# Performance work log

Hardware: AMD Instinct MI355X
Metric: run time of the kernel (lower is better)

Reference implementation:

```python
import jax, jax.numpy as jnp
import numpy as np

DIM = 2048
N_HEADS = 16
N_KV_HEADS = 8
HEAD_DIM = DIM // N_HEADS  # 128
N_REP = N_HEADS // N_KV_HEADS
BATCH = 2
SEQ = 2048
CHUNK = 128  # chunked-parallel causal linear attention; SEQ % CHUNK == 0


def _make_freqs_cis(seq_len, head_dim, theta=10000.0):
    freqs = 1.0 / (theta ** (np.arange(0, head_dim, 2, dtype=np.float32) / head_dim))
    t = np.arange(seq_len, dtype=np.float32)
    ang = np.outer(t, freqs)  # [S, D/2]
    return jnp.asarray(np.stack([np.cos(ang), np.sin(ang)], axis=-1))  # [S, D/2, 2]


def setup_inputs() -> dict:
    key = jax.random.key(0)
    ks = jax.random.split(key, 5)
    x = jax.random.normal(ks[0], (BATCH, SEQ, DIM), dtype=jnp.float32)
    freqs_cis = _make_freqs_cis(SEQ, HEAD_DIM)
    s = 0.02
    wq = s * jax.random.normal(ks[1], (N_HEADS * HEAD_DIM, DIM), dtype=jnp.float32)
    wk = s * jax.random.normal(ks[2], (N_KV_HEADS * HEAD_DIM, DIM), dtype=jnp.float32)
    wv = s * jax.random.normal(ks[3], (N_KV_HEADS * HEAD_DIM, DIM), dtype=jnp.float32)
    wo = s * jax.random.normal(ks[4], (DIM, N_HEADS * HEAD_DIM), dtype=jnp.float32)
    return {"x": x, "freqs_cis": freqs_cis, "wq": wq, "wk": wk, "wv": wv, "wo": wo}


def _apply_rotary(x, freqs_cis):
    # x: [B, S, H, D]; freqs_cis: [S, D/2, 2] (cos, sin). Llama pairing: (x0,x1),(x2,x3),...
    B, S, H, D = x.shape
    xr = x.reshape(B, S, H, D // 2, 2)
    x0, x1 = xr[..., 0], xr[..., 1]
    c = freqs_cis[None, :, None, :, 0]
    s = freqs_cis[None, :, None, :, 1]
    o0 = x0 * c - x1 * s
    o1 = x0 * s + x1 * c
    return jnp.stack([o0, o1], axis=-1).reshape(B, S, H, D)


def _causal_linear_attention(q, k, v):
    # q, k, v: [B, H, S, D]; output_i = q_i @ sum_{j<=i} k_j^T v_j
    B, H, S, D = q.shape
    q = jax.nn.softmax(q * (D ** -0.5), axis=-1)  # softmax over feature dim
    k = jax.nn.softmax(k, axis=2)                 # softmax over sequence dim (as in source)
    Nc = S // CHUNK
    qc = q.reshape(B, H, Nc, CHUNK, D)
    kc = k.reshape(B, H, Nc, CHUNK, D)
    vc = v.reshape(B, H, Nc, CHUNK, D)
    # per-chunk KV outer-product sums: [B, H, Nc, D, D]
    kv = jnp.einsum('bhncd,bhnce->bhnde', kc, vc)
    cum = jnp.cumsum(kv, axis=2)
    cum_excl = jnp.concatenate([jnp.zeros_like(cum[:, :, :1]), cum[:, :, :-1]], axis=2)
    inter = jnp.einsum('bhncd,bhnde->bhnce', qc, cum_excl)
    scores = jnp.einsum('bhncd,bhnmd->bhncm', qc, kc)  # [B,H,Nc,C,C]
    mask = jnp.tril(jnp.ones((CHUNK, CHUNK), dtype=bool))
    scores = jnp.where(mask, scores, jnp.zeros((), dtype=scores.dtype))
    intra = jnp.einsum('bhncm,bhnme->bhnce', scores, vc)
    return (inter + intra).reshape(B, H, S, D)


def reference(x, freqs_cis, wq, wk, wv, wo):
    B, S, _ = x.shape
    xq = (x @ wq.T).reshape(B, S, N_HEADS, HEAD_DIM)
    xk = (x @ wk.T).reshape(B, S, N_KV_HEADS, HEAD_DIM)
    xv = (x @ wv.T).reshape(B, S, N_KV_HEADS, HEAD_DIM)
    xq = _apply_rotary(xq, freqs_cis)
    xk = _apply_rotary(xk, freqs_cis)
    # repeat_kv: each kv head repeated N_REP consecutive times
    keys = jnp.repeat(xk, N_REP, axis=2)
    values = jnp.repeat(xv, N_REP, axis=2)
    q = jnp.transpose(xq, (0, 2, 1, 3))
    k = jnp.transpose(keys, (0, 2, 1, 3))
    v = jnp.transpose(values, (0, 2, 1, 3))
    out = _causal_linear_attention(q, k, v)  # [B, H, S, D]
    out = jnp.transpose(out, (0, 2, 1, 3)).reshape(B, S, N_HEADS * HEAD_DIM)
    return out @ wo.T
```

## Files before the change

kernel.cpp:

```cpp
#include <hip/hip_runtime.h>
#include <math.h>

#define DIMV 2048
#define NHEAD 16
#define NKV 8
#define HD 128
#define BATCH 2
#define SEQ 2048
#define CHUNK 128
#define NCHUNK 16
#define MTOK 4096
#define KVD (NKV * HD)

typedef _Float16 half8_t __attribute__((ext_vector_type(8)));
typedef _Float16 half4_t __attribute__((ext_vector_type(4)));
typedef _Float16 half2_t __attribute__((ext_vector_type(2)));
typedef float f32x4 __attribute__((ext_vector_type(4)));

#define GLOBAL_AS __attribute__((address_space(1)))
#define LDS_AS __attribute__((address_space(3)))

#define BARX() __builtin_amdgcn_s_barrier()
#define WAITL(n) asm volatile("s_waitcnt lgkmcnt(" #n ")" ::: "memory")
#define WAITVM(n) asm volatile("s_waitcnt vmcnt(" #n ")" ::: "memory")

__global__ __launch_bounds__(256) void cast_all(const float* __restrict__ x,
                                                const float* __restrict__ wq,
                                                const float* __restrict__ wk,
                                                const float* __restrict__ wv,
                                                const float* __restrict__ wo,
                                                _Float16* __restrict__ xh,
                                                _Float16* __restrict__ wqkvh,
                                                _Float16* __restrict__ woh) {
  long i = (long)(blockIdx.x * 256 + threadIdx.x) * 8;
  const float* src;
  _Float16* dst;
  long off;
  if (i < 8388608)        { src = x;  dst = xh;              off = 0; }
  else if (i < 12582912)  { src = wq; dst = wqkvh;           off = 8388608; }
  else if (i < 14680064)  { src = wk; dst = wqkvh + 4194304; off = 12582912; }
  else if (i < 16777216)  { src = wv; dst = wqkvh + 6291456; off = 14680064; }
  else                    { src = wo; dst = woh;             off = 16777216; }
  long e = i - off;
  float4 a = *(const float4*)&src[e];
  float4 b = *(const float4*)&src[e + 4];
  half8_t h = {(_Float16)a.x, (_Float16)a.y, (_Float16)a.z, (_Float16)a.w,
               (_Float16)b.x, (_Float16)b.y, (_Float16)b.z, (_Float16)b.w};
  *(half8_t*)&dst[e] = h;
}

__global__ __launch_bounds__(256) void transpose_fc(const float* __restrict__ fc,
                                                    float* __restrict__ fcT) {
  __shared__ float T[64][65];
  int s0 = blockIdx.x * 64, d0 = blockIdx.y * 64;
  int t = threadIdx.x;
  int r = t >> 4, c4 = (t & 15) * 4;
#pragma unroll
  for (int p = 0; p < 4; ++p) {
    int sr = p * 16 + r;
    float4 v = *(const float4*)&fc[(size_t)(s0 + sr) * 128 + d0 + c4];
    T[sr][c4] = v.x; T[sr][c4 + 1] = v.y; T[sr][c4 + 2] = v.z; T[sr][c4 + 3] = v.w;
  }
  __syncthreads();
#pragma unroll
  for (int p = 0; p < 4; ++p) {
    int dr = p * 16 + r;
    float4 v = make_float4(T[c4][dr], T[c4 + 1][dr], T[c4 + 2][dr], T[c4 + 3][dr]);
    *(float4*)&fcT[(size_t)(d0 + dr) * SEQ + s0 + c4] = v;
  }
}

#define STG_A(bb, kk, i, k0)                                                      \
  __builtin_amdgcn_global_load_lds(                                               \
      (const GLOBAL_AS void*)(A + aoff + (size_t)(i) * 128 * 2048 + (k0) + (kk) * 32), \
      (LDS_AS void*)(As + ((bb) * 2 + (kk)) * 8192 + (i) * 4096 + wave * 512), 16, 0, 0)
#define STG_B(bb, kk, i, k0)                                                      \
  __builtin_amdgcn_global_load_lds(                                               \
      (const GLOBAL_AS void*)(B + boff + (size_t)(i) * 128 * 2048 + (k0) + (kk) * 32), \
      (LDS_AS void*)(Bs + ((bb) * 2 + (kk)) * 8192 + (i) * 4096 + wave * 512), 16, 0, 0)

#define LDA_F(bb, kk, ih) do {                                                    \
    const _Float16* pA_ = As + ((bb) * 2 + (kk)) * 8192 +                         \
                          (wr * 128 + (ih) * 64 + m16) * 32 + pseg8;              \
    af[0] = *(const half8_t*)(pA_);                                               \
    af[1] = *(const half8_t*)(pA_ + 512);                                         \
    af[2] = *(const half8_t*)(pA_ + 1024);                                        \
    af[3] = *(const half8_t*)(pA_ + 1536);                                        \
  } while (0)
#define LDB_F(bb, kk) do {                                                        \
    const _Float16* pB_ = Bs + ((bb) * 2 + (kk)) * 8192 +                         \
                          (wc * 64 + m16) * 32 + pseg8;                           \
    bf[0] = *(const half8_t*)(pB_);                                               \
    bf[1] = *(const half8_t*)(pB_ + 512);                                         \
    bf[2] = *(const half8_t*)(pB_ + 1024);                                        \
    bf[3] = *(const half8_t*)(pB_ + 1536);                                        \
  } while (0)

#define MMX(ih) do {                                                              \
    _Pragma("unroll")                                                             \
    for (int i_ = 0; i_ < 4; ++i_)                                                \
      _Pragma("unroll")                                                           \
      for (int j_ = 0; j_ < 4; ++j_)                                              \
        acc[(ih) * 4 + i_][j_] = __builtin_amdgcn_mfma_f32_16x16x32_f16(          \
            af[i_], bf[j_], acc[(ih) * 4 + i_][j_], 0, 0, 0);                     \
  } while (0)

#define KTILE(bb, k0, DS1, DS2, DS3, DS4, VA, VB) do {                            \
  half8_t af[4], bf[4];                                                           \
                                                           \
  LDA_F(bb, 0, 0); LDB_F(bb, 0);                                                  \
  if (DS1) { STG_A(1 - (bb), 1, 0, (k0) + 64); STG_A(1 - (bb), 1, 1, (k0) + 64); } \
  BARX(); WAITL(0);                                                               \
  __builtin_amdgcn_s_setprio(1); MMX(0); __builtin_amdgcn_s_setprio(0);           \
  BARX();                                                                         \
                                                \
  LDA_F(bb, 0, 1);                                                                \
  if (DS2) { STG_B(1 - (bb), 1, 0, (k0) + 64); STG_B(1 - (bb), 1, 1, (k0) + 64); } \
  WAITVM(VA);                                                                     \
  BARX(); WAITL(0);                                                               \
  __builtin_amdgcn_s_setprio(1); MMX(1); __builtin_amdgcn_s_setprio(0);           \
  BARX();                                                                         \
                                                           \
  LDA_F(bb, 1, 0); LDB_F(bb, 1);                                                  \
  if (DS3) { STG_A(bb, 0, 0, (k0) + 128); STG_A(bb, 0, 1, (k0) + 128); }          \
  BARX(); WAITL(0);                                                               \
  __builtin_amdgcn_s_setprio(1); MMX(0); __builtin_amdgcn_s_setprio(0);           \
  BARX();                                                                         \
                                                \
  LDA_F(bb, 1, 1);                                                                \
  if (DS4) { STG_B(bb, 0, 0, (k0) + 128); STG_B(bb, 0, 1, (k0) + 128); }          \
  WAITVM(VB);                                                                     \
  BARX(); WAITL(0);                                                               \
  __builtin_amdgcn_s_setprio(1); MMX(1); __builtin_amdgcn_s_setprio(0);           \
  BARX();                                                                         \
} while (0)

__global__ __launch_bounds__(512, 2) void hgemm_qkv_8p(const _Float16* __restrict__ A,
                                                       const _Float16* __restrict__ B,
                                                       const float* __restrict__ fc,
                                                       _Float16* __restrict__ qh,
                                                       _Float16* __restrict__ kT,
                                                       _Float16* __restrict__ vT) {
  const int K = 2048;
  __shared__ _Float16 As[32768];
  __shared__ _Float16 Bs[32768];
  __shared__ float qsum[4][256];

  const int tid = threadIdx.x;
  const int lane = tid & 63;
  const int wave = tid >> 6;
  const int wr = wave >> 2;
  const int wc = wave & 3;
  const int m16 = lane & 15, quad = lane >> 4;
  const int row0 = blockIdx.y * 256, col0 = blockIdx.x * 256;
  const int pseg8 = (quad ^ ((m16 >> 1) & 3)) * 8;

  const int r_ld = tid >> 2;
  const int sseg = (tid & 3) ^ ((tid >> 3) & 3);
  const size_t aoff = (size_t)(row0 + r_ld) * K + sseg * 8;
  const size_t boff = (size_t)(col0 + r_ld) * K + sseg * 8;

  f32x4 acc[8][4];
#pragma unroll
  for (int m = 0; m < 8; ++m)
#pragma unroll
    for (int j = 0; j < 4; ++j) acc[m][j] = (f32x4){0.f, 0.f, 0.f, 0.f};

  STG_A(0, 0, 0, 0); STG_A(0, 0, 1, 0); STG_B(0, 0, 0, 0); STG_B(0, 0, 1, 0);
  STG_A(0, 1, 0, 0); STG_A(0, 1, 1, 0); STG_B(0, 1, 0, 0); STG_B(0, 1, 1, 0);
  STG_A(1, 0, 0, 64); STG_A(1, 0, 1, 64); STG_B(1, 0, 0, 64); STG_B(1, 0, 1, 64);
  WAITVM(8);
  BARX();

  for (int t = 0; t < 30; t += 2) {
    KTILE(0, t * 64,      1, 1, 1, 1, 8, 8);
    KTILE(1, t * 64 + 64, 1, 1, 1, 1, 8, 8);
  }
  KTILE(0, 1920, 1, 1, 0, 0, 8, 4);
  KTILE(1, 1984, 0, 0, 0, 0, 0, 0);

  if (col0 < 2048) {
    const float sc = 0.08838834764831845f;
    float psum[8][4];
#pragma unroll
    for (int m = 0; m < 8; ++m)
#pragma unroll
      for (int r = 0; r < 4; ++r) psum[m][r] = 0.f;
#pragma unroll
    for (int m = 0; m < 8; ++m)
#pragma unroll
      for (int j = 0; j < 4; ++j) {
        int dl2 = (wc * 64 + j * 16 + m16) & 126;
#pragma unroll
        for (int r = 0; r < 4; ++r) {
          float val = acc[m][j][r];
          float par = __shfl_xor(val, 1);
          int row_l = wr * 128 + (m >> 2) * 64 + (m & 3) * 16 + quad * 4 + r;
          int s_tok = (row0 + row_l) & (SEQ - 1);
          float2 cs = *(const float2*)&fc[(size_t)s_tok * 128 + dl2];
          float o = val * cs.x + par * ((m16 & 1) ? cs.y : -cs.y);
          float e = __expf(o * sc);
          acc[m][j][r] = e;
          psum[m][r] += e;
        }
      }
#pragma unroll
    for (int mm = 1; mm < 16; mm <<= 1)
#pragma unroll
      for (int m = 0; m < 8; ++m)
#pragma unroll
        for (int r = 0; r < 4; ++r) psum[m][r] += __shfl_xor(psum[m][r], mm);
    if (m16 == 0) {
#pragma unroll
      for (int m = 0; m < 8; ++m)
#pragma unroll
        for (int r = 0; r < 4; ++r) {
          int row_l = wr * 128 + (m >> 2) * 64 + (m & 3) * 16 + quad * 4 + r;
          qsum[wc][row_l] = psum[m][r];
        }
    }
    __syncthreads();
#pragma unroll
    for (int m = 0; m < 8; ++m)
#pragma unroll
      for (int r = 0; r < 4; ++r) {
        int row_l = wr * 128 + (m >> 2) * 64 + (m & 3) * 16 + quad * 4 + r;
        psum[m][r] = 1.f / (qsum[wc & 2][row_l] + qsum[(wc & 2) | 1][row_l]);
      }
#pragma unroll
    for (int m = 0; m < 8; ++m)
#pragma unroll
      for (int j = 0; j < 4; ++j) {
        int col = col0 + wc * 64 + j * 16 + m16;
#pragma unroll
        for (int r = 0; r < 4; ++r) {
          int row_l = wr * 128 + (m >> 2) * 64 + (m & 3) * 16 + quad * 4 + r;
          qh[(size_t)(row0 + row_l) * DIMV + col] = (_Float16)(acc[m][j][r] * psum[m][r]);
        }
      }
  } else {
#pragma unroll
    for (int m = 0; m < 8; ++m)
#pragma unroll
      for (int j = 0; j < 4; ++j) {
        int col = col0 + wc * 64 + j * 16 + m16;
        int rowb = row0 + wr * 128 + (m >> 2) * 64 + (m & 3) * 16 + quad * 4;
        half4_t hv = {(_Float16)acc[m][j][0], (_Float16)acc[m][j][1],
                      (_Float16)acc[m][j][2], (_Float16)acc[m][j][3]};
        if (col0 < 3072) {
          *(half4_t*)&kT[(size_t)(col - 2048) * MTOK + rowb] = hv;
        } else {
          *(half4_t*)&vT[(size_t)(col - 3072) * MTOK + rowb] = hv;
        }
      }
  }
}

#define STGBT(bb, kk, k0) do {                                                    \
  __builtin_amdgcn_global_load_lds(                                               \
      (const GLOBAL_AS void*)(A + abase + (k0) + (kk) * 32),                      \
      (LDS_AS void*)(As + ((bb) * 2 + (kk)) * 4096 + wave * 512), 16, 0, 0);      \
  __builtin_amdgcn_global_load_lds(                                               \
      (const GLOBAL_AS void*)(B + bbase + (k0) + (kk) * 32),                      \
      (LDS_AS void*)(Bs + ((bb) * 2 + (kk)) * 8192 + wave * 512), 16, 0, 0);      \
  __builtin_amdgcn_global_load_lds(                                               \
      (const GLOBAL_AS void*)(B + bbase + (size_t)128 * 2048 + (k0) + (kk) * 32), \
      (LDS_AS void*)(Bs + ((bb) * 2 + (kk)) * 8192 + 4096 + wave * 512), 16, 0, 0);\
} while (0)

#define PHASE_BT(bb, kk, SEN, sbb, skk, sk0, VM) do {                             \
  WAITVM(VM);                                                                     \
  BARX();                                                                         \
  half8_t af[4], bf[4];                                                           \
  const _Float16* pA_ = As + ((bb) * 2 + (kk)) * 4096 +                           \
                        (wr * 64 + m16) * 32 + pseg8;                             \
  const _Float16* pB_ = Bs + ((bb) * 2 + (kk)) * 8192 +                           \
                        (wc * 64 + m16) * 32 + pseg8;                             \
  af[0] = *(const half8_t*)(pA_);        af[1] = *(const half8_t*)(pA_ + 512);    \
  af[2] = *(const half8_t*)(pA_ + 1024); af[3] = *(const half8_t*)(pA_ + 1536);   \
  bf[0] = *(const half8_t*)(pB_);        bf[1] = *(const half8_t*)(pB_ + 512);    \
  bf[2] = *(const half8_t*)(pB_ + 1024); bf[3] = *(const half8_t*)(pB_ + 1536);   \
  if (SEN) STGBT(sbb, skk, sk0);                                                  \
  WAITL(0);                                                                       \
  __builtin_amdgcn_s_setprio(1);                                                  \
  _Pragma("unroll")                                                               \
  for (int i_ = 0; i_ < 4; ++i_)                                                  \
    _Pragma("unroll")                                                             \
    for (int j_ = 0; j_ < 4; ++j_)                                                \
      acc[i_][j_] = __builtin_amdgcn_mfma_f32_16x16x32_f16(                       \
          af[i_], bf[j_], acc[i_][j_], 0, 0, 0);                                  \
  __builtin_amdgcn_s_setprio(0);                                                  \
} while (0)

__global__ __launch_bounds__(512, 2) void hgemm_bt_8p(const _Float16* __restrict__ A,
                                                      const _Float16* __restrict__ B,
                                                      float* __restrict__ C) {
  const int K = 2048, N = 2048;
  __shared__ _Float16 As[16384];
  __shared__ _Float16 Bs[32768];

  const int tid = threadIdx.x;
  const int lane = tid & 63;
  const int wave = tid >> 6;
  const int wr = wave >> 2;
  const int wc = wave & 3;
  const int m16 = lane & 15, quad = lane >> 4;
  const int row0 = blockIdx.y * 128, col0 = blockIdx.x * 256;
  const int pseg8 = (quad ^ ((m16 >> 1) & 3)) * 8;

  const int r_ld = tid >> 2;
  const int sseg = (tid & 3) ^ ((tid >> 3) & 3);
  const size_t abase = (size_t)(row0 + r_ld) * K + sseg * 8;
  const size_t bbase = (size_t)(col0 + r_ld) * K + sseg * 8;

  f32x4 acc[4][4];
#pragma unroll
  for (int i = 0; i < 4; ++i)
#pragma unroll
    for (int j = 0; j < 4; ++j) acc[i][j] = (f32x4){0.f, 0.f, 0.f, 0.f};

  STGBT(0, 0, 0); STGBT(0, 1, 0); STGBT(1, 0, 64);

  for (int t = 0; t < 30; ++t) {
    const int bb = t & 1;
    const int k0 = t * 64;
    PHASE_BT(bb, 0, 1, bb ^ 1, 1, k0 + 64, 6);
    PHASE_BT(bb, 1, 1, bb, 0, k0 + 128, 6);
  }
  PHASE_BT(0, 0, 1, 1, 1, 1984, 6);
  PHASE_BT(0, 1, 0, 0, 0, 0, 6);
  PHASE_BT(1, 0, 0, 0, 0, 0, 3);
  PHASE_BT(1, 1, 0, 0, 0, 0, 0);

#pragma unroll
  for (int i = 0; i < 4; ++i)
#pragma unroll
    for (int j = 0; j < 4; ++j) {
      int col = col0 + wc * 64 + j * 16 + m16;
      int rowb = row0 + wr * 64 + i * 16 + quad * 4;
#pragma unroll
      for (int r = 0; r < 4; ++r) C[(size_t)(rowb + r) * N + col] = acc[i][j][r];
    }
}

__global__ __launch_bounds__(256) void k_rope_softmax_T(_Float16* __restrict__ kT,
                                                        const float* __restrict__ fcT) {
  int bi = blockIdx.x;
  int b = bi & 1, pr = bi >> 1;
  int d0 = pr * 2, dl = d0 & 127;
  int t = threadIdx.x;
  size_t r0 = (size_t)d0 * MTOK + b * SEQ + t * 8;
  size_t r1 = r0 + MTOK;
  half8_t x0v = *(half8_t*)&kT[r0];
  half8_t x1v = *(half8_t*)&kT[r1];
  int s8 = t * 8;
  float4 ca = *(const float4*)&fcT[(size_t)dl * SEQ + s8];
  float4 cb = *(const float4*)&fcT[(size_t)dl * SEQ + s8 + 4];
  float4 sa = *(const float4*)&fcT[(size_t)(dl + 1) * SEQ + s8];
  float4 sb = *(const float4*)&fcT[(size_t)(dl + 1) * SEQ + s8 + 4];
  float cc[8] = {ca.x, ca.y, ca.z, ca.w, cb.x, cb.y, cb.z, cb.w};
  float ss[8] = {sa.x, sa.y, sa.z, sa.w, sb.x, sb.y, sb.z, sb.w};
  float e0[8], e1[8];
  float sum0 = 0.f, sum1 = 0.f;
#pragma unroll
  for (int j = 0; j < 8; ++j) {
    float x0 = (float)x0v[j], x1 = (float)x1v[j];
    float o0 = x0 * cc[j] - x1 * ss[j];
    float o1 = x0 * ss[j] + x1 * cc[j];
    e0[j] = expf(o0); e1[j] = expf(o1);
    sum0 += e0[j]; sum1 += e1[j];
  }
#pragma unroll
  for (int off = 1; off < 64; off <<= 1) {
    sum0 += __shfl_xor(sum0, off);
    sum1 += __shfl_xor(sum1, off);
  }
  __shared__ float red[8];
  if ((t & 63) == 0) { red[(t >> 6) * 2] = sum0; red[(t >> 6) * 2 + 1] = sum1; }
  __syncthreads();
  float S0 = red[0] + red[2] + red[4] + red[6];
  float S1 = red[1] + red[3] + red[5] + red[7];
  float i0 = 1.f / S0, i1 = 1.f / S1;
  half8_t w0, w1;
#pragma unroll
  for (int j = 0; j < 8; ++j) {
    w0[j] = (_Float16)(e0[j] * i0);
    w1[j] = (_Float16)(e1[j] * i1);
  }
  *(half8_t*)&kT[r0] = w0;
  *(half8_t*)&kT[r1] = w1;
}

__global__ __launch_bounds__(256) void transpose_k(const _Float16* __restrict__ kT,
                                                   _Float16* __restrict__ kh) {
  __shared__ _Float16 T[64][65];
  int t0 = blockIdx.x * 64, d0 = blockIdx.y * 64;
  int t = threadIdx.x;
  int r = t >> 3, c8 = (t & 7) * 8;
#pragma unroll
  for (int p = 0; p < 2; ++p) {
    int dr = p * 32 + r;
    half8_t v = *(const half8_t*)&kT[(size_t)(d0 + dr) * MTOK + t0 + c8];
#pragma unroll
    for (int j = 0; j < 8; ++j) T[c8 + j][dr] = v[j];
  }
  __syncthreads();
#pragma unroll
  for (int p = 0; p < 2; ++p) {
    int tr = p * 32 + r;
    half8_t v;
#pragma unroll
    for (int j = 0; j < 8; ++j) v[j] = T[tr][c8 + j];
    *(half8_t*)&kh[(size_t)(t0 + tr) * KVD + d0 + c8] = v;
  }
}

__global__ __launch_bounds__(256) void kv_chunk_mfma(const _Float16* __restrict__ vT,
                                                     const _Float16* __restrict__ kT,
                                                     float* __restrict__ kvT) {
  __shared__ _Float16 As[2][128 * 32];
  __shared__ _Float16 Bs[2][128 * 32];
  int bi = blockIdx.x;
  int n = bi & 15, kvh = (bi >> 4) & 7, b = bi >> 7;
  int tok0 = b * SEQ + n * CHUNK;
  const int tid = threadIdx.x;
  const int lane = tid & 63;
  const int wave = tid >> 6;
  const int wr = wave & 1, wc = wave >> 1;
  const int m16 = lane & 15, quad = lane >> 4;
  const int qsw8 = (quad ^ ((m16 >> 1) & 3)) * 8;

  f32x4 acc[4][4];
#pragma unroll
  for (int i = 0; i < 4; ++i)
#pragma unroll
    for (int j = 0; j < 4; ++j) acc[i][j] = (f32x4){0.f, 0.f, 0.f, 0.f};

  const int r_ld = tid >> 2;
  const int sseg = (tid & 3) ^ ((tid >> 3) & 3);
  const size_t a_base = (size_t)(kvh * HD + r_ld) * MTOK + tok0 + sseg * 8;

#pragma unroll
  for (int i = 0; i < 2; ++i) {
    __builtin_amdgcn_global_load_lds(
        (const GLOBAL_AS void*)(vT + a_base + (size_t)i * 64 * MTOK),
        (LDS_AS void*)(&As[0][0] + i * 2048 + wave * 512), 16, 0, 0);
    __builtin_amdgcn_global_load_lds(
        (const GLOBAL_AS void*)(kT + a_base + (size_t)i * 64 * MTOK),
        (LDS_AS void*)(&Bs[0][0] + i * 2048 + wave * 512), 16, 0, 0);
  }

#pragma unroll
  for (int s = 0; s < 4; ++s) {
    WAITVM(0);
    BARX();
    if (s < 3) {
      const int k0 = (s + 1) * 32;
      const int bb = (s + 1) & 1;
#pragma unroll
      for (int i = 0; i < 2; ++i) {
        __builtin_amdgcn_global_load_lds(
            (const GLOBAL_AS void*)(vT + a_base + (size_t)i * 64 * MTOK + k0),
            (LDS_AS void*)(&As[bb][0] + i * 2048 + wave * 512), 16, 0, 0);
        __builtin_amdgcn_global_load_lds(
            (const GLOBAL_AS void*)(kT + a_base + (size_t)i * 64 * MTOK + k0),
            (LDS_AS void*)(&Bs[bb][0] + i * 2048 + wave * 512), 16, 0, 0);
      }
    }
    const _Float16* ra = &As[s & 1][0];
    const _Float16* rb = &Bs[s & 1][0];
    half8_t af[4], bf[4];
#pragma unroll
    for (int i = 0; i < 4; ++i) {
      af[i] = *(const half8_t*)&ra[(wr * 64 + i * 16 + m16) * 32 + qsw8];
      bf[i] = *(const half8_t*)&rb[(wc * 64 + i * 16 + m16) * 32 + qsw8];
    }
#pragma unroll
    for (int i = 0; i < 4; ++i)
#pragma unroll
      for (int j = 0; j < 4; ++j)
        acc[i][j] = __builtin_amdgcn_mfma_f32_16x16x32_f16(af[i], bf[j], acc[i][j], 0, 0, 0);
  }
#pragma unroll
  for (int i = 0; i < 4; ++i)
#pragma unroll
    for (int j = 0; j < 4; ++j) {
      int col = wc * 64 + j * 16 + m16;
      int rowb = wr * 64 + i * 16 + quad * 4;
#pragma unroll
      for (int r = 0; r < 4; ++r)
        kvT[(size_t)bi * 16384 + (size_t)(rowb + r) * 128 + col] = acc[i][j][r];
    }
}

__global__ __launch_bounds__(256) void cumsum_h(const float* __restrict__ kvT,
                                                _Float16* __restrict__ cumh) {
  int gid = blockIdx.x * 256 + threadIdx.x;
  int bk = gid >> 14, idx = gid & 16383;
  size_t base = (size_t)bk * NCHUNK * 16384 + idx;
  float run = 0.f;
#pragma unroll
  for (int n = 0; n < NCHUNK; ++n) {
    cumh[base + (size_t)n * 16384] = (_Float16)run;
    run += kvT[base + (size_t)n * 16384];
  }
}

__global__ __launch_bounds__(256) void attn_fused(const _Float16* __restrict__ qh,
                                                  const _Float16* __restrict__ kh,
                                                  const _Float16* __restrict__ cumh,
                                                  const _Float16* __restrict__ vT,
                                                  _Float16* __restrict__ ath) {
  __shared__ _Float16 Qs[128 * 128];
  __shared__ _Float16 Bs[2][128 * 32];
  __shared__ _Float16 Ss[128 * 128];
  int bi = blockIdx.x;
  int n = bi & 15, h = (bi >> 4) & 15, b = bi >> 8;
  int kvh = h >> 1;
  int tok0 = b * SEQ + n * CHUNK;
  const int tid = threadIdx.x;
  const int lane = tid & 63;
  const int wave = tid >> 6;
  const int wr = wave & 1, wc = wave >> 1;
  const int m16 = lane & 15, quad = lane >> 4;
  const int qsw8 = (quad ^ ((m16 >> 1) & 3)) * 8;
  const int r_ld = tid >> 2;
  const int sseg = (tid & 3) ^ ((tid >> 3) & 3);

  f32x4 acc[4][4];
#pragma unroll
  for (int i = 0; i < 4; ++i)
#pragma unroll
    for (int j = 0; j < 4; ++j) acc[i][j] = (f32x4){0.f, 0.f, 0.f, 0.f};

  const int qrow = tid >> 4;
  const int qsl = (tid & 15) ^ (qrow & 7);
  const size_t qsrc = (size_t)(tok0 + qrow) * DIMV + h * HD + qsl * 8;
#pragma unroll
  for (int p = 0; p < 8; ++p)
    __builtin_amdgcn_global_load_lds(
        (const GLOBAL_AS void*)(qh + qsrc + (size_t)p * 16 * DIMV),
        (LDS_AS void*)(Qs + p * 2048 + wave * 512), 16, 0, 0);

  const size_t kbase = (size_t)(tok0 + r_ld) * KVD + kvh * HD + sseg * 8;
  const size_t cbase = ((size_t)((b * 8 + kvh) * 16 + n)) * 16384 + (size_t)r_ld * 128 + sseg * 8;
  const size_t vbase = (size_t)(kvh * HD + r_ld) * MTOK + tok0 + sseg * 8;

#pragma unroll
  for (int i = 0; i < 2; ++i)
    __builtin_amdgcn_global_load_lds(
        (const GLOBAL_AS void*)(kh + kbase + (size_t)i * 64 * KVD),
        (LDS_AS void*)(&Bs[0][0] + i * 2048 + wave * 512), 16, 0, 0);

#pragma unroll
  for (int s = 0; s < 12; ++s) {
    WAITVM(0);
    BARX();
    if (s < 11) {
      const int sn = s + 1;
      _Float16* dstB = &Bs[sn & 1][0];
      if (sn < 4) {
        const int k0 = sn * 32;
#pragma unroll
        for (int i = 0; i < 2; ++i)
          __builtin_amdgcn_global_load_lds(
              (const GLOBAL_AS void*)(kh + kbase + (size_t)i * 64 * KVD + k0),
              (LDS_AS void*)(dstB + i * 2048 + wave * 512), 16, 0, 0);
      } else if (sn < 8) {
        const int k0 = (sn - 4) * 32;
#pragma unroll
        for (int i = 0; i < 2; ++i)
          __builtin_amdgcn_global_load_lds(
              (const GLOBAL_AS void*)(cumh + cbase + (size_t)i * 64 * 128 + k0),
              (LDS_AS void*)(dstB + i * 2048 + wave * 512), 16, 0, 0);
      } else {
        const int k0 = (sn - 8) * 32;
#pragma unroll
        for (int i = 0; i < 2; ++i)
          __builtin_amdgcn_global_load_lds(
              (const GLOBAL_AS void*)(vT + vbase + (size_t)i * 64 * MTOK + k0),
              (LDS_AS void*)(dstB + i * 2048 + wave * 512), 16, 0, 0);
      }
    }
    half8_t af[4], bf[4];
    const _Float16* rb = &Bs[s & 1][0];
#pragma unroll
    for (int i = 0; i < 4; ++i)
      bf[i] = *(const half8_t*)&rb[(wc * 64 + i * 16 + m16) * 32 + qsw8];
    if (s < 8) {
      const int sl4 = (s & 3) * 4;
#pragma unroll
      for (int i = 0; i < 4; ++i) {
        int row = wr * 64 + i * 16 + m16;
        af[i] = *(const half8_t*)&Qs[row * 128 + ((sl4 + quad) ^ (m16 & 7)) * 8];
      }
    } else {
      const int sl4 = (s - 8) * 4;
#pragma unroll
      for (int i = 0; i < 4; ++i) {
        int row = wr * 64 + i * 16 + m16;
        af[i] = *(const half8_t*)&Ss[row * 128 + ((sl4 + quad) ^ (m16 & 7)) * 8];
      }
    }
#pragma unroll
    for (int i = 0; i < 4; ++i)
#pragma unroll
      for (int j = 0; j < 4; ++j)
        acc[i][j] = __builtin_amdgcn_mfma_f32_16x16x32_f16(af[i], bf[j], acc[i][j], 0, 0, 0);
    if (s == 3) {
#pragma unroll
      for (int i = 0; i < 4; ++i)
#pragma unroll
        for (int j = 0; j < 4; ++j) {
          int col = wc * 64 + j * 16 + m16;
          int rowb = wr * 64 + i * 16 + quad * 4;
#pragma unroll
          for (int r = 0; r < 4; ++r) {
            int row = rowb + r;
            float v = (col <= row) ? acc[i][j][r] : 0.f;
            int sp = (col >> 3) ^ (row & 7);
            Ss[row * 128 + sp * 8 + (col & 7)] = (_Float16)v;
          }
          acc[i][j] = (f32x4){0.f, 0.f, 0.f, 0.f};
        }
      WAITL(0);
    }
  }

#pragma unroll
  for (int i = 0; i < 4; ++i)
#pragma unroll
    for (int j = 0; j < 4; ++j) {
      int col = wc * 64 + j * 16 + m16;
      int rowb = wr * 64 + i * 16 + quad * 4;
#pragma unroll
      for (int r = 0; r < 4; ++r)
        ath[(size_t)(tok0 + rowb + r) * DIMV + h * HD + col] = (_Float16)acc[i][j][r];
    }
}

extern "C" void kernel_launch(void* const* d_in, const int* in_sizes, int n_in,
                              void* d_out, int out_size, void* d_ws, size_t ws_size,
                              hipStream_t stream) {
  const float* x  = (const float*)d_in[0];
  const float* fc = (const float*)d_in[1];
  const float* wq = (const float*)d_in[2];
  const float* wk = (const float*)d_in[3];
  const float* wv = (const float*)d_in[4];
  const float* wo = (const float*)d_in[5];
  float* out = (float*)d_out;

  char* p = (char*)d_ws;
  _Float16* xh    = (_Float16*)p;  p += 16777216;
  _Float16* wqkvh = (_Float16*)p;  p += 16777216;
  _Float16* woh   = (_Float16*)p;  p += 8388608;
  _Float16* qh    = (_Float16*)p;  p += 16777216;
  _Float16* kT    = (_Float16*)p;  p += 8388608;
  _Float16* kh    = (_Float16*)p;  p += 8388608;
  _Float16* vT    = (_Float16*)p;  p += 8388608;
  float*    kvT   = (float*)p;     p += 16777216;
  _Float16* cumh  = (_Float16*)p;  p += 8388608;
  _Float16* ath   = (_Float16*)p;  p += 16777216;
  float*    fcT   = (float*)p;     p += 1048576;

  cast_all<<<10240, 256, 0, stream>>>(x, wq, wk, wv, wo, xh, wqkvh, woh);
  transpose_fc<<<dim3(32, 2), 256, 0, stream>>>(fc, fcT);

  hgemm_qkv_8p<<<dim3(16, 16), 512, 0, stream>>>(xh, wqkvh, fc, qh, kT, vT);

  k_rope_softmax_T<<<1024, 256, 0, stream>>>(kT, fcT);
  transpose_k<<<dim3(64, 16), 256, 0, stream>>>(kT, kh);

  kv_chunk_mfma<<<256, 256, 0, stream>>>(vT, kT, kvT);
  cumsum_h<<<1024, 256, 0, stream>>>(kvT, cumh);
  attn_fused<<<512, 256, 0, stream>>>(qh, kh, cumh, vT, ath);

  hgemm_bt_8p<<<dim3(8, 32), 512, 0, stream>>>(ath, woh, out);
}
```

Baseline: 287.2 us.

## Fuse kernels: transpose into cast, rope-softmax with K transpose, KV sums with cumsum

The fc transpose moves into extra blocks of the cast kernel. The K rotary/softmax and K transpose become one LDS-staged kernel writing both layouts. The per-chunk KV outer products and the fp32 cumsum merge into a kernel that keeps running sums in registers across chunks and writes the fp16 prefix directly. This drops three launches and the fp32 kvT round trip. The cost is much lower parallelism: k_finalize runs only 128 blocks and kv_cum only 64 blocks, each looping serially over 16 chunks.

```diff
diff --git a/kernel.cpp b/kernel.cpp
--- a/kernel.cpp
+++ b/kernel.cpp
@@ -31,7 +31,30 @@
                                                 const float* __restrict__ wo,
                                                 _Float16* __restrict__ xh,
                                                 _Float16* __restrict__ wqkvh,
-                                                _Float16* __restrict__ woh) {
+                                                _Float16* __restrict__ woh,
+                                                const float* __restrict__ fc,
+                                                float* __restrict__ fcT) {
+  __shared__ float T[64][65];
+  if (blockIdx.x >= 10240) {
+    int q = blockIdx.x - 10240;
+    int s0 = (q & 31) * 64, d0 = (q >> 5) * 64;
+    int t = threadIdx.x;
+    int r = t >> 4, c4 = (t & 15) * 4;
+#pragma unroll
+    for (int p = 0; p < 4; ++p) {
+      int sr = p * 16 + r;
+      float4 v = *(const float4*)&fc[(size_t)(s0 + sr) * 128 + d0 + c4];
+      T[sr][c4] = v.x; T[sr][c4 + 1] = v.y; T[sr][c4 + 2] = v.z; T[sr][c4 + 3] = v.w;
+    }
+    __syncthreads();
+#pragma unroll
+    for (int p = 0; p < 4; ++p) {
+      int dr = p * 16 + r;
+      float4 v = make_float4(T[c4][dr], T[c4 + 1][dr], T[c4 + 2][dr], T[c4 + 3][dr]);
+      *(float4*)&fcT[(size_t)(d0 + dr) * SEQ + s0 + c4] = v;
+    }
+    return;
+  }
   long i = (long)(blockIdx.x * 256 + threadIdx.x) * 8;
   const float* src;
   _Float16* dst;
@@ -49,27 +72,6 @@
   *(half8_t*)&dst[e] = h;
 }
 
-__global__ __launch_bounds__(256) void transpose_fc(const float* __restrict__ fc,
-                                                    float* __restrict__ fcT) {
-  __shared__ float T[64][65];
-  int s0 = blockIdx.x * 64, d0 = blockIdx.y * 64;
-  int t = threadIdx.x;
-  int r = t >> 4, c4 = (t & 15) * 4;
-#pragma unroll
-  for (int p = 0; p < 4; ++p) {
-    int sr = p * 16 + r;
-    float4 v = *(const float4*)&fc[(size_t)(s0 + sr) * 128 + d0 + c4];
-    T[sr][c4] = v.x; T[sr][c4 + 1] = v.y; T[sr][c4 + 2] = v.z; T[sr][c4 + 3] = v.w;
-  }
-  __syncthreads();
-#pragma unroll
-  for (int p = 0; p < 4; ++p) {
-    int dr = p * 16 + r;
-    float4 v = make_float4(T[c4][dr], T[c4 + 1][dr], T[c4 + 2][dr], T[c4 + 3][dr]);
-    *(float4*)&fcT[(size_t)(d0 + dr) * SEQ + s0 + c4] = v;
-  }
-}
-
 #define STG_A(bb, kk, i, k0)                                                      \
   __builtin_amdgcn_global_load_lds(                                               \
       (const GLOBAL_AS void*)(A + aoff + (size_t)(i) * 128 * 2048 + (k0) + (kk) * 32), \
@@ -107,26 +109,22 @@
 
 #define KTILE(bb, k0, DS1, DS2, DS3, DS4, VA, VB) do {                            \
   half8_t af[4], bf[4];                                                           \
-                                                           \
   LDA_F(bb, 0, 0); LDB_F(bb, 0);                                                  \
   if (DS1) { STG_A(1 - (bb), 1, 0, (k0) + 64); STG_A(1 - (bb), 1, 1, (k0) + 64); } \
   BARX(); WAITL(0);                                                               \
   __builtin_amdgcn_s_setprio(1); MMX(0); __builtin_amdgcn_s_setprio(0);           \
   BARX();                                                                         \
-                                                \
   LDA_F(bb, 0, 1);                                                                \
   if (DS2) { STG_B(1 - (bb), 1, 0, (k0) + 64); STG_B(1 - (bb), 1, 1, (k0) + 64); } \
   WAITVM(VA);                                                                     \
   BARX(); WAITL(0);                                                               \
   __builtin_amdgcn_s_setprio(1); MMX(1); __builtin_amdgcn_s_setprio(0);           \
   BARX();                                                                         \
-                                                           \
   LDA_F(bb, 1, 0); LDB_F(bb, 1);                                                  \
   if (DS3) { STG_A(bb, 0, 0, (k0) + 128); STG_A(bb, 0, 1, (k0) + 128); }          \
   BARX(); WAITL(0);                                                               \
   __builtin_amdgcn_s_setprio(1); MMX(0); __builtin_amdgcn_s_setprio(0);           \
   BARX();                                                                         \
-                                                \
   LDA_F(bb, 1, 1);                                                                \
   if (DS4) { STG_B(bb, 0, 0, (k0) + 128); STG_B(bb, 0, 1, (k0) + 128); }          \
   WAITVM(VB);                                                                     \
@@ -343,166 +341,179 @@
     }
 }
 
-__global__ __launch_bounds__(256) void k_rope_softmax_T(_Float16* __restrict__ kT,
-                                                        const float* __restrict__ fcT) {
-  int bi = blockIdx.x;
-  int b = bi & 1, pr = bi >> 1;
-  int d0 = pr * 2, dl = d0 & 127;
-  int t = threadIdx.x;
-  size_t r0 = (size_t)d0 * MTOK + b * SEQ + t * 8;
-  size_t r1 = r0 + MTOK;
-  half8_t x0v = *(half8_t*)&kT[r0];
-  half8_t x1v = *(half8_t*)&kT[r1];
-  int s8 = t * 8;
-  float4 ca = *(const float4*)&fcT[(size_t)dl * SEQ + s8];
-  float4 cb = *(const float4*)&fcT[(size_t)dl * SEQ + s8 + 4];
-  float4 sa = *(const float4*)&fcT[(size_t)(dl + 1) * SEQ + s8];
-  float4 sb = *(const float4*)&fcT[(size_t)(dl + 1) * SEQ + s8 + 4];
-  float cc[8] = {ca.x, ca.y, ca.z, ca.w, cb.x, cb.y, cb.z, cb.w};
-  float ss[8] = {sa.x, sa.y, sa.z, sa.w, sb.x, sb.y, sb.z, sb.w};
-  float e0[8], e1[8];
-  float sum0 = 0.f, sum1 = 0.f;
-#pragma unroll
-  for (int j = 0; j < 8; ++j) {
-    float x0 = (float)x0v[j], x1 = (float)x1v[j];
-    float o0 = x0 * cc[j] - x1 * ss[j];
-    float o1 = x0 * ss[j] + x1 * cc[j];
-    e0[j] = expf(o0); e1[j] = expf(o1);
-    sum0 += e0[j]; sum1 += e1[j];
-  }
-#pragma unroll
-  for (int off = 1; off < 64; off <<= 1) {
-    sum0 += __shfl_xor(sum0, off);
-    sum1 += __shfl_xor(sum1, off);
-  }
-  __shared__ float red[8];
-  if ((t & 63) == 0) { red[(t >> 6) * 2] = sum0; red[(t >> 6) * 2 + 1] = sum1; }
+__global__ __launch_bounds__(256) void k_finalize(_Float16* __restrict__ kT,
+                                                  _Float16* __restrict__ kh,
+                                                  const float* __restrict__ fcT) {
+  __shared__ float T[16][2052];
+  __shared__ float red[64];
+  __shared__ float inv_s[16];
+  const int bi = blockIdx.x;
+  const int b = bi & 1, dg = bi >> 1;
+  const int d0 = dg * 16;
+  const int t = threadIdx.x;
+  const int wv = t >> 6;
+  const int s8 = t * 8;
+
+#pragma unroll
+  for (int pr = 0; pr < 8; ++pr) {
+    const int da = d0 + pr * 2;
+    const int dla = da & 127;
+    size_t r0 = (size_t)da * MTOK + b * SEQ + s8;
+    half8_t x0v = *(const half8_t*)&kT[r0];
+    half8_t x1v = *(const half8_t*)&kT[r0 + MTOK];
+    float4 ca = *(const float4*)&fcT[(size_t)dla * SEQ + s8];
+    float4 cb = *(const float4*)&fcT[(size_t)dla * SEQ + s8 + 4];
+    float4 sa = *(const float4*)&fcT[(size_t)(dla + 1) * SEQ + s8];
+    float4 sb = *(const float4*)&fcT[(size_t)(dla + 1) * SEQ + s8 + 4];
+    float cc[8] = {ca.x, ca.y, ca.z, ca.w, cb.x, cb.y, cb.z, cb.w};
+    float ss[8] = {sa.x, sa.y, sa.z, sa.w, sb.x, sb.y, sb.z, sb.w};
+    float sum0 = 0.f, sum1 = 0.f;
+#pragma unroll
+    for (int j = 0; j < 8; ++j) {
+      float x0 = (float)x0v[j], x1 = (float)x1v[j];
+      float o0 = x0 * cc[j] - x1 * ss[j];
+      float o1 = x0 * ss[j] + x1 * cc[j];
+      float e0 = expf(o0), e1 = expf(o1);
+      T[pr * 2][s8 + j] = e0;
+      T[pr * 2 + 1][s8 + j] = e1;
+      sum0 += e0; sum1 += e1;
+    }
+#pragma unroll
+    for (int off = 1; off < 64; off <<= 1) {
+      sum0 += __shfl_xor(sum0, off);
+      sum1 += __shfl_xor(sum1, off);
+    }
+    if ((t & 63) == 0) {
+      red[pr * 8 + wv * 2] = sum0;
+      red[pr * 8 + wv * 2 + 1] = sum1;
+    }
+  }
   __syncthreads();
-  float S0 = red[0] + red[2] + red[4] + red[6];
-  float S1 = red[1] + red[3] + red[5] + red[7];
-  float i0 = 1.f / S0, i1 = 1.f / S1;
-  half8_t w0, w1;
-#pragma unroll
-  for (int j = 0; j < 8; ++j) {
-    w0[j] = (_Float16)(e0[j] * i0);
-    w1[j] = (_Float16)(e1[j] * i1);
-  }
-  *(half8_t*)&kT[r0] = w0;
-  *(half8_t*)&kT[r1] = w1;
+  if (t < 16) {
+    int pr = t >> 1, par = t & 1;
+    float den = red[pr * 8 + par] + red[pr * 8 + 2 + par] +
+                red[pr * 8 + 4 + par] + red[pr * 8 + 6 + par];
+    inv_s[t] = 1.f / den;
+  }
+  __syncthreads();
+
+#pragma unroll
+  for (int d = 0; d < 16; ++d) {
+    float iv = inv_s[d];
+    half8_t w;
+#pragma unroll
+    for (int j = 0; j < 8; ++j) w[j] = (_Float16)(T[d][s8 + j] * iv);
+    *(half8_t*)&kT[(size_t)(d0 + d) * MTOK + b * SEQ + s8] = w;
+  }
+  float iv[16];
+#pragma unroll
+  for (int d = 0; d < 16; ++d) iv[d] = inv_s[d];
+#pragma unroll
+  for (int jj = 0; jj < 8; ++jj) {
+    int tok = jj * 256 + t;
+    half8_t wa, wb;
+#pragma unroll
+    for (int d = 0; d < 8; ++d) {
+      wa[d] = (_Float16)(T[d][tok] * iv[d]);
+      wb[d] = (_Float16)(T[d + 8][tok] * iv[d + 8]);
+    }
+    size_t o = (size_t)(b * SEQ + tok) * KVD + d0;
+    *(half8_t*)&kh[o] = wa;
+    *(half8_t*)&kh[o + 8] = wb;
+  }
 }
 
-__global__ __launch_bounds__(256) void transpose_k(const _Float16* __restrict__ kT,
-                                                   _Float16* __restrict__ kh) {
-  __shared__ _Float16 T[64][65];
-  int t0 = blockIdx.x * 64, d0 = blockIdx.y * 64;
-  int t = threadIdx.x;
-  int r = t >> 3, c8 = (t & 7) * 8;
-#pragma unroll
-  for (int p = 0; p < 2; ++p) {
-    int dr = p * 32 + r;
-    half8_t v = *(const half8_t*)&kT[(size_t)(d0 + dr) * MTOK + t0 + c8];
-#pragma unroll
-    for (int j = 0; j < 8; ++j) T[c8 + j][dr] = v[j];
-  }
-  __syncthreads();
-#pragma unroll
-  for (int p = 0; p < 2; ++p) {
-    int tr = p * 32 + r;
-    half8_t v;
-#pragma unroll
-    for (int j = 0; j < 8; ++j) v[j] = T[tr][c8 + j];
-    *(half8_t*)&kh[(size_t)(t0 + tr) * KVD + d0 + c8] = v;
-  }
-}
-
-__global__ __launch_bounds__(256) void kv_chunk_mfma(const _Float16* __restrict__ vT,
-                                                     const _Float16* __restrict__ kT,
-                                                     float* __restrict__ kvT) {
-  __shared__ _Float16 As[2][128 * 32];
-  __shared__ _Float16 Bs[2][128 * 32];
-  int bi = blockIdx.x;
-  int n = bi & 15, kvh = (bi >> 4) & 7, b = bi >> 7;
-  int tok0 = b * SEQ + n * CHUNK;
+#define KVSTG(buf, n) do {                                                        \
+  const size_t t0_ = (size_t)b * SEQ + (size_t)(n) * CHUNK;                       \
+  _Pragma("unroll")                                                               \
+  for (int i_ = 0; i_ < 4; ++i_) {                                                \
+    __builtin_amdgcn_global_load_lds(                                             \
+        (const GLOBAL_AS void*)(vT + (size_t)(e0 + i_ * 16 + rhi) * MTOK + t0_ + slog * 8), \
+        (LDS_AS void*)(Vs + (buf) * 8192 + i_ * 2048 + wave * 512), 16, 0, 0);    \
+    __builtin_amdgcn_global_load_lds(                                             \
+        (const GLOBAL_AS void*)(kT + (size_t)(d0 + i_ * 16 + rhi) * MTOK + t0_ + slog * 8), \
+        (LDS_AS void*)(Ks + (buf) * 8192 + i_ * 2048 + wave * 512), 16, 0, 0);    \
+  }                                                                               \
+} while (0)
+
+__global__ __launch_bounds__(256) void kv_cum(const _Float16* __restrict__ vT,
+                                              const _Float16* __restrict__ kT,
+                                              _Float16* __restrict__ cumh) {
+  __shared__ _Float16 Vs[2 * 8192];
+  __shared__ _Float16 Ks[2 * 8192];
+  const int bi = blockIdx.x;
+  const int eh = bi & 1, dh = (bi >> 1) & 1, kvh = (bi >> 2) & 7, b = bi >> 5;
+  const int e0 = kvh * HD + eh * 64;
+  const int d0 = kvh * HD + dh * 64;
   const int tid = threadIdx.x;
   const int lane = tid & 63;
   const int wave = tid >> 6;
-  const int wr = wave & 1, wc = wave >> 1;
+  const int wr = wave >> 1, wcd = wave & 1;
   const int m16 = lane & 15, quad = lane >> 4;
-  const int qsw8 = (quad ^ ((m16 >> 1) & 3)) * 8;
-
-  f32x4 acc[4][4];
-#pragma unroll
-  for (int i = 0; i < 4; ++i)
-#pragma unroll
-    for (int j = 0; j < 4; ++j) acc[i][j] = (f32x4){0.f, 0.f, 0.f, 0.f};
-
-  const int r_ld = tid >> 2;
-  const int sseg = (tid & 3) ^ ((tid >> 3) & 3);
-  const size_t a_base = (size_t)(kvh * HD + r_ld) * MTOK + tok0 + sseg * 8;
-
-#pragma unroll
-  for (int i = 0; i < 2; ++i) {
-    __builtin_amdgcn_global_load_lds(
-        (const GLOBAL_AS void*)(vT + a_base + (size_t)i * 64 * MTOK),
-        (LDS_AS void*)(&As[0][0] + i * 2048 + wave * 512), 16, 0, 0);
-    __builtin_amdgcn_global_load_lds(
-        (const GLOBAL_AS void*)(kT + a_base + (size_t)i * 64 * MTOK),
-        (LDS_AS void*)(&Bs[0][0] + i * 2048 + wave * 512), 16, 0, 0);
-  }
-
-#pragma unroll
-  for (int s = 0; s < 4; ++s) {
-    WAITVM(0);
+
+  const int rhi = tid >> 4;
+  const int slog = (tid & 15) ^ rhi;
+
+  const size_t cbase0 = ((size_t)(b * 8 + kvh) * 16) * 16384;
+  const int erel = eh * 64 + wr * 32;
+  const int drel = dh * 64 + wcd * 32;
+
+  f32x4 run[2][2];
+#pragma unroll
+  for (int i = 0; i < 2; ++i)
+#pragma unroll
+    for (int j = 0; j < 2; ++j) run[i][j] = (f32x4){0.f, 0.f, 0.f, 0.f};
+
+  KVSTG(0, 0);
+  KVSTG(1, 1);
+
+#pragma unroll
+  for (int n = 0; n < NCHUNK; ++n) {
+    if (n < 15) { WAITVM(8); } else { WAITVM(0); }
     BARX();
-    if (s < 3) {
-      const int k0 = (s + 1) * 32;
-      const int bb = (s + 1) & 1;
+    {
+      size_t cb = cbase0 + (size_t)n * 16384;
+#pragma unroll
+      for (int i = 0; i < 2; ++i)
+#pragma unroll
+        for (int j = 0; j < 2; ++j)
+#pragma unroll
+          for (int r = 0; r < 4; ++r) {
+            int e = erel + i * 16 + quad * 4 + r;
+            int d = drel + j * 16 + m16;
+            cumh[cb + (size_t)e * 128 + d] = (_Float16)run[i][j][r];
+          }
+    }
+    const _Float16* rv = Vs + (n & 1) * 8192;
+    const _Float16* rk = Ks + (n & 1) * 8192;
+    f32x4 acc[2][2];
+#pragma unroll
+    for (int i = 0; i < 2; ++i)
+#pragma unroll
+      for (int j = 0; j < 2; ++j) acc[i][j] = (f32x4){0.f, 0.f, 0.f, 0.f};
+#pragma unroll
+    for (int ks = 0; ks < 4; ++ks) {
+      half8_t af[2], bf[2];
 #pragma unroll
       for (int i = 0; i < 2; ++i) {
-        __builtin_amdgcn_global_load_lds(
-            (const GLOBAL_AS void*)(vT + a_base + (size_t)i * 64 * MTOK + k0),
-            (LDS_AS void*)(&As[bb][0] + i * 2048 + wave * 512), 16, 0, 0);
-        __builtin_amdgcn_global_load_lds(
-            (const GLOBAL_AS void*)(kT + a_base + (size_t)i * 64 * MTOK + k0),
-            (LDS_AS void*)(&Bs[bb][0] + i * 2048 + wave * 512), 16, 0, 0);
-      }
-    }
-    const _Float16* ra = &As[s & 1][0];
-    const _Float16* rb = &Bs[s & 1][0];
-    half8_t af[4], bf[4];
-#pragma unroll
-    for (int i = 0; i < 4; ++i) {
-      af[i] = *(const half8_t*)&ra[(wr * 64 + i * 16 + m16) * 32 + qsw8];
-      bf[i] = *(const half8_t*)&rb[(wc * 64 + i * 16 + m16) * 32 + qsw8];
-    }
-#pragma unroll
-    for (int i = 0; i < 4; ++i)
-#pragma unroll
-      for (int j = 0; j < 4; ++j)
-        acc[i][j] = __builtin_amdgcn_mfma_f32_16x16x32_f16(af[i], bf[j], acc[i][j], 0, 0, 0);
-  }
-#pragma unroll
-  for (int i = 0; i < 4; ++i)
-#pragma unroll
-    for (int j = 0; j < 4; ++j) {
-      int col = wc * 64 + j * 16 + m16;
-      int rowb = wr * 64 + i * 16 + quad * 4;
-#pragma unroll
-      for (int r = 0; r < 4; ++r)
-        kvT[(size_t)bi * 16384 + (size_t)(rowb + r) * 128 + col] = acc[i][j][r];
-    }
-}
-
-__global__ __launch_bounds__(256) void cumsum_h(const float* __restrict__ kvT,
-                                                _Float16* __restrict__ cumh) {
-  int gid = blockIdx.x * 256 + threadIdx.x;
-  int bk = gid >> 14, idx = gid & 16383;
-  size_t base = (size_t)bk * NCHUNK * 16384 + idx;
-  float run = 0.f;
-#pragma unroll
-  for (int n = 0; n < NCHUNK; ++n) {
-    cumh[base + (size_t)n * 16384] = (_Float16)run;
-    run += kvT[base + (size_t)n * 16384];
+        int rowv = wr * 32 + i * 16 + m16;
+        int rowk = wcd * 32 + i * 16 + m16;
+        int ps = (ks * 4 + quad) ^ m16;
+        af[i] = *(const half8_t*)&rv[rowv * 128 + ps * 8];
+        bf[i] = *(const half8_t*)&rk[rowk * 128 + ps * 8];
+      }
+#pragma unroll
+      for (int i = 0; i < 2; ++i)
+#pragma unroll
+        for (int j = 0; j < 2; ++j)
+          acc[i][j] = __builtin_amdgcn_mfma_f32_16x16x32_f16(af[i], bf[j], acc[i][j], 0, 0, 0);
+    }
+#pragma unroll
+    for (int i = 0; i < 2; ++i)
+#pragma unroll
+      for (int j = 0; j < 2; ++j) run[i][j] += acc[i][j];
+    BARX();
+    if (n < 14) KVSTG(n & 1, n + 2);
   }
 }
 
@@ -662,17 +673,16 @@
   _Float16* cumh  = (_Float16*)p;  p += 8388608;
   _Float16* ath   = (_Float16*)p;  p += 16777216;
   float*    fcT   = (float*)p;     p += 1048576;
-
-  cast_all<<<10240, 256, 0, stream>>>(x, wq, wk, wv, wo, xh, wqkvh, woh);
-  transpose_fc<<<dim3(32, 2), 256, 0, stream>>>(fc, fcT);
+  (void)kvT;
+
+  cast_all<<<10304, 256, 0, stream>>>(x, wq, wk, wv, wo, xh, wqkvh, woh, fc, fcT);
 
   hgemm_qkv_8p<<<dim3(16, 16), 512, 0, stream>>>(xh, wqkvh, fc, qh, kT, vT);
 
-  k_rope_softmax_T<<<1024, 256, 0, stream>>>(kT, fcT);
-  transpose_k<<<dim3(64, 16), 256, 0, stream>>>(kT, kh);
-
-  kv_chunk_mfma<<<256, 256, 0, stream>>>(vT, kT, kvT);
-  cumsum_h<<<1024, 256, 0, stream>>>(kvT, cumh);
+  k_finalize<<<128, 256, 0, stream>>>(kT, kh, fcT);
+
+  kv_cum<<<64, 256, 0, stream>>>(vT, kT, cumh);
+
   attn_fused<<<512, 256, 0, stream>>>(qh, kh, cumh, vT, ath);
 
   hgemm_bt_8p<<<dim3(8, 32), 512, 0, stream>>>(ath, woh, out);
```

Measured after the change: 292.5 us. Within noise of the previous version (+1.9%).
